# Performance work log

Hardware: AMD Instinct MI355X
Metric: run time of the kernel (lower is better)

Reference implementation:

```python
import jax, jax.numpy as jnp
import numpy as np

N_EMBD = 1024
N_HEAD = 16


def setup_inputs() -> dict:
    key = jax.random.key(0)
    k1, k2, k3 = jax.random.split(key, 3)
    x = jax.random.normal(k1, (4, 2048, N_EMBD), dtype=jnp.float32)
    w_attn = jax.random.normal(k2, (N_EMBD, 3 * N_EMBD), dtype=jnp.float32) * (N_EMBD ** -0.5)
    w_proj = jax.random.normal(k3, (N_EMBD, N_EMBD), dtype=jnp.float32) * (N_EMBD ** -0.5)
    return {"x": x, "w_attn": w_attn, "w_proj": w_proj}


def reference(x, w_attn, w_proj):
    B, T, C = x.shape
    H = N_HEAD
    D = C // H  # head dim
    qkv = x @ w_attn  # [B,T,3C]
    q, k, v = jnp.split(qkv, 3, axis=-1)
    # [B,T,C] -> [B,H,T,D]
    q = q.reshape(B, T, H, D).transpose(0, 2, 1, 3)
    k = k.reshape(B, T, H, D).transpose(0, 2, 1, 3)
    v = v.reshape(B, T, H, D).transpose(0, 2, 1, 3)
    scale = 1.0 / jnp.sqrt(jnp.asarray(D, dtype=x.dtype))
    att = jnp.einsum('bhqd,bhkd->bhqk', q, k) * scale  # [B,H,T,T]
    causal = jnp.tril(jnp.ones((T, T), dtype=bool))
    att = jnp.where(causal, att, jnp.asarray(-jnp.inf, dtype=att.dtype))
    att = jax.nn.softmax(att, axis=-1)
    y = jnp.einsum('bhqk,bhkd->bhqd', att, v)  # [B,H,T,D]
    y = y.transpose(0, 2, 1, 3).reshape(B, T, C)
    return y @ w_proj
```

## Files before the change

kernel.cpp:

```cpp
#include <hip/hip_runtime.h>
#include <math.h>


typedef unsigned short ushort_t;
typedef __attribute__((ext_vector_type(8))) short bf16x8;
typedef __attribute__((ext_vector_type(4))) float f32x4;

#define MFMA16(a, b, c) __builtin_amdgcn_mfma_f32_16x16x32_bf16((a), (b), (c), 0, 0, 0)

#define CP_ASYNC16(lds, gp)                                                        \
    __builtin_amdgcn_global_load_lds(                                              \
        (const __attribute__((address_space(1))) void*)(gp),                       \
        (__attribute__((address_space(3))) void*)(lds), 16, 0, 0)

#define SCALE2 0.1803368801111204f

__device__ __forceinline__ ushort_t bf16r(float x) {
    unsigned int u = __float_as_uint(x);
    u += 0x7FFFu + ((u >> 16) & 1u);
    return (ushort_t)(u >> 16);
}


__global__ __launch_bounds__(256) void cast_f32_bf16(const float4* __restrict__ src,
                                                     ushort4* __restrict__ dst) {
    int i = blockIdx.x * 256 + threadIdx.x;
    float4 v = src[i];
    ushort4 o;
    o.x = bf16r(v.x); o.y = bf16r(v.y); o.z = bf16r(v.z); o.w = bf16r(v.w);
    dst[i] = o;
}

__global__ __launch_bounds__(256) void transpose_cast(const float* __restrict__ src,
                                                      ushort_t* __restrict__ dst,
                                                      int R, int Cc) {
    __shared__ float tile[32][33];
    const int tx = threadIdx.x, ty = threadIdx.y;
    const int c0 = blockIdx.x * 32, r0 = blockIdx.y * 32;
#pragma unroll
    for (int i = 0; i < 4; ++i)
        tile[ty + i * 8][tx] = src[(size_t)(r0 + ty + i * 8) * Cc + c0 + tx];
    __syncthreads();
#pragma unroll
    for (int i = 0; i < 4; ++i)
        dst[(size_t)(c0 + ty + i * 8) * R + r0 + tx] = bf16r(tile[tx][ty + i * 8]);
}

__global__ __launch_bounds__(256)
void gemm_bf16(const ushort_t* __restrict__ A, const ushort_t* __restrict__ Bt,
               int K, int mode,
               ushort_t* __restrict__ Qh, ushort_t* __restrict__ Kh,
               ushort_t* __restrict__ Vt, float* __restrict__ Cout) {
    __shared__ ushort_t As[2][128 * 32];
    __shared__ ushort_t Bs[2][128 * 32];
    const int tid = threadIdx.x;
    const int l = tid & 63, w = tid >> 6;
    const int lm = l & 15, lq = l >> 4;
    const int wm = w >> 1, wn = w & 1;
    const int row0 = blockIdx.y * 128, col0 = blockIdx.x * 128;
    const f32x4 zero4 = {0.f, 0.f, 0.f, 0.f};
    const int lqs8 = (lq ^ ((lm >> 1) & 3)) * 8;

    f32x4 acc[4][4];
#pragma unroll
    for (int i = 0; i < 4; ++i)
#pragma unroll
        for (int j = 0; j < 4; ++j) acc[i][j] = zero4;

    const int srow = tid >> 2, slot = tid & 3;
    const int soff = (slot ^ ((srow >> 1) & 3)) * 8;
    const ushort_t* ga0 = A + (size_t)(row0 + srow) * K + soff;
    const ushort_t* ga1 = ga0 + (size_t)64 * K;
    const ushort_t* gb0 = Bt + (size_t)(col0 + srow) * K + soff;
    const ushort_t* gb1 = gb0 + (size_t)64 * K;

    const int aoffb = (wm * 64 + lm) * 32 + lqs8;
    const int boffb = (wn * 64 + lm) * 32 + lqs8;

    auto prefetch = [&](int k0, int dbuf) {
        CP_ASYNC16(&As[dbuf][tid * 8], ga0 + k0);
        CP_ASYNC16(&As[dbuf][(tid + 256) * 8], ga1 + k0);
        CP_ASYNC16(&Bs[dbuf][tid * 8], gb0 + k0);
        CP_ASYNC16(&Bs[dbuf][(tid + 256) * 8], gb1 + k0);
    };

    prefetch(0, 0);
    const int niter = K >> 5;
    for (int it = 0; it < niter; ++it) {
        const int buf = it & 1;
        __syncthreads();
        if (it + 1 < niter) prefetch((it + 1) << 5, buf ^ 1);

        bf16x8 af[4], bfr[4];
#pragma unroll
        for (int i = 0; i < 4; ++i)
            af[i] = *(const bf16x8*)(As[buf] + aoffb + i * (16 * 32));
#pragma unroll
        for (int j = 0; j < 4; ++j)
            bfr[j] = *(const bf16x8*)(Bs[buf] + boffb + j * (16 * 32));
#pragma unroll
        for (int i = 0; i < 4; ++i)
#pragma unroll
            for (int j = 0; j < 4; ++j)
                acc[i][j] = MFMA16(af[i], bfr[j], acc[i][j]);
    }

#pragma unroll
    for (int i = 0; i < 4; ++i) {
#pragma unroll
        for (int j = 0; j < 4; ++j) {
#pragma unroll
            for (int reg = 0; reg < 4; ++reg) {
                const int rr = row0 + wm * 64 + i * 16 + lq * 4 + reg;
                const int cc = col0 + wn * 64 + j * 16 + lm;
                const float v = acc[i][j][reg];
                if (mode == 1) {
                    Cout[(size_t)rr * 1024 + cc] = v;
                } else {
                    const int b = rr >> 11, t = rr & 2047;
                    if (cc < 1024) {
                        const int h = cc >> 6, d = cc & 63;
                        Qh[((size_t)(b * 16 + h) * 2048 + t) * 64 + d] =
                            bf16r(v * SCALE2);
                    } else if (cc < 2048) {
                        const int c2 = cc - 1024, h = c2 >> 6, d = c2 & 63;
                        Kh[((size_t)(b * 16 + h) * 2048 + t) * 64 + d] = bf16r(v);
                    } else {
                        const int c2 = cc - 2048, h = c2 >> 6, d = c2 & 63;
                        Vt[((size_t)(b * 16 + h) * 64 + d) * 2048 + t] = bf16r(v);
                    }
                }
            }
        }
    }
}

__global__ __launch_bounds__(256, 4)
void attn_mfma(const ushort_t* __restrict__ Qh, const ushort_t* __restrict__ Kh,
               const ushort_t* __restrict__ Vt, ushort_t* __restrict__ Y) {
    __shared__ ushort_t Ks[2][4096];
    __shared__ ushort_t Vs[2][4096];
    __shared__ ushort_t Ps[4][1024];
    const int tid = threadIdx.x, l = tid & 63, w = tid >> 6;
    const int lm = l & 15, lq = l >> 4;
    const int bh = blockIdx.x;
    const int pr = blockIdx.y;
    const int qbA = pr, qbB = 31 - pr;
    const int b = bh >> 4, h = bh & 15;
    const f32x4 zero4 = {0.f, 0.f, 0.f, 0.f};
    const short oneb = (short)0x3F80;
    const bf16x8 onesf = {oneb, oneb, oneb, oneb, oneb, oneb, oneb, oneb};
    const int lqs8 = (lq ^ ((lm >> 1) & 3)) * 8;

    bf16x8 qf[2][2];
    {
        const ushort_t* qA = Qh + ((size_t)bh * 2048 + qbA * 64 + w * 16 + lm) * 64 + lq * 8;
        const ushort_t* qB = Qh + ((size_t)bh * 2048 + qbB * 64 + w * 16 + lm) * 64 + lq * 8;
        qf[0][0] = *(const bf16x8*)(qA);
        qf[0][1] = *(const bf16x8*)(qA + 32);
        qf[1][0] = *(const bf16x8*)(qB);
        qf[1][1] = *(const bf16x8*)(qB + 32);
    }

    f32x4 O[2][4], Ol[2];
#pragma unroll
    for (int q = 0; q < 2; ++q) {
        Ol[q] = zero4;
#pragma unroll
        for (int i = 0; i < 4; ++i) O[q][i] = zero4;
    }

    const int srow = tid >> 2, slot = tid & 3;
    const int srcoff = ((slot ^ ((srow >> 1) & 3)) * 8);
    const ushort_t* gKr = Kh + ((size_t)bh * 2048 + srow) * 64 + srcoff;
    const ushort_t* gVr = Vt + ((size_t)bh * 64 + srow) * 2048 + srcoff;
    ushort_t* Pw = Ps[w];

    auto prefetch = [&](int jbn, int dbuf) {
        const ushort_t* gk = gKr + (size_t)jbn * 4096;
        const ushort_t* gv = gVr + jbn * 64;
        CP_ASYNC16(&Ks[dbuf][tid * 8], gk);
        CP_ASYNC16(&Ks[dbuf][2048 + tid * 8], gk + 32);
        CP_ASYNC16(&Vs[dbuf][tid * 8], gv);
        CP_ASYNC16(&Vs[dbuf][2048 + tid * 8], gv + 32);
    };

    auto process = [&](const bf16x8 (&kf)[4][2], const ushort_t* Vb,
                       const bf16x8 (&qfr)[2], f32x4 (&Or)[4], f32x4& Olr,
                       bool diag) {
        f32x4 sf[4];
#pragma unroll
        for (int n = 0; n < 4; ++n) {
            f32x4 s_acc = zero4;
            s_acc = MFMA16(qfr[0], kf[n][0], s_acc);
            s_acc = MFMA16(qfr[1], kf[n][1], s_acc);
            sf[n] = s_acc;
        }

        float p[4][4];
#pragma unroll
        for (int n = 0; n < 4; ++n)
#pragma unroll
            for (int reg = 0; reg < 4; ++reg)
                p[n][reg] = __builtin_amdgcn_exp2f(sf[n][reg]);
        if (diag) {
#pragma unroll
            for (int n = 0; n < 4; ++n) {
                const int key = n * 16 + lm;
#pragma unroll
                for (int reg = 0; reg < 4; ++reg) {
                    const int qloc = w * 16 + lq * 4 + reg;
                    if (key > qloc) p[n][reg] = 0.f;
                }
            }
        }

#pragma unroll
        for (int n = 0; n < 4; ++n) {
            const int ch = n >> 1, nn = n & 1;
#pragma unroll
            for (int reg = 0; reg < 4; ++reg) {
                const int r = lq * 4 + reg;
                const int ss = (nn * 2 + (lm >> 3)) ^ ((2 * lq + (reg >> 1)) & 3);
                const unsigned int u = __float_as_uint(p[n][reg]) + 0x8000u;
                Pw[ch * 512 + r * 32 + ss * 8 + (lm & 7)] = (ushort_t)(u >> 16);
            }
        }
        const bf16x8 pf0 = *(const bf16x8*)(Pw + lm * 32 + lqs8);
        const bf16x8 pf1 = *(const bf16x8*)(Pw + 512 + lm * 32 + lqs8);

#pragma unroll
        for (int dn = 0; dn < 4; ++dn) {
            const bf16x8 vf0 = *(const bf16x8*)(Vb + (dn * 16 + lm) * 32 + lqs8);
            const bf16x8 vf1 = *(const bf16x8*)(Vb + 2048 + (dn * 16 + lm) * 32 + lqs8);
            Or[dn] = MFMA16(pf0, vf0, Or[dn]);
            Or[dn] = MFMA16(pf1, vf1, Or[dn]);
        }
        Olr = MFMA16(pf0, onesf, Olr);
        Olr = MFMA16(pf1, onesf, Olr);
    };

    prefetch(0, 0);
    for (int jb = 0; jb <= qbB; ++jb) {
        const int buf = jb & 1;
        __syncthreads();
        if (jb < qbB) prefetch(jb + 1, buf ^ 1);

        const ushort_t* Kb = Ks[buf];
        const ushort_t* Vb = Vs[buf];
        bf16x8 kf[4][2];
#pragma unroll
        for (int n = 0; n < 4; ++n) {
            kf[n][0] = *(const bf16x8*)(Kb + (n * 16 + lm) * 32 + lqs8);
            kf[n][1] = *(const bf16x8*)(Kb + 2048 + (n * 16 + lm) * 32 + lqs8);
        }

        process(kf, Vb, qf[1], O[1], Ol[1], jb == qbB);
        if (jb <= qbA)
            process(kf, Vb, qf[0], O[0], Ol[0], jb == qbA);
    }

#pragma unroll
    for (int qs = 0; qs < 2; ++qs) {
        const int tq = (qs ? qbB : qbA) * 64;
#pragma unroll
        for (int reg = 0; reg < 4; ++reg) {
            const float inv = 1.f / Ol[qs][reg];
            const size_t row = (size_t)b * 2048 + tq + w * 16 + lq * 4 + reg;
#pragma unroll
            for (int dn = 0; dn < 4; ++dn)
                Y[row * 1024 + h * 64 + dn * 16 + lm] = bf16r(O[qs][dn][reg] * inv);
        }
    }
}


extern "C" void kernel_launch(void* const* d_in, const int* in_sizes, int n_in,
                              void* d_out, int out_size, void* d_ws, size_t ws_size,
                              hipStream_t stream) {
    const float* x      = (const float*)d_in[0];
    const float* w_attn = (const float*)d_in[1];
    const float* w_proj = (const float*)d_in[2];
    float* out = (float*)d_out;

    char* ws = (char*)d_ws;
    ushort_t* xb   = (ushort_t*)(ws);
    ushort_t* watT = (ushort_t*)(ws + 16777216);
    ushort_t* wpjT = (ushort_t*)(ws + 23068672);
    ushort_t* Qh   = (ushort_t*)(ws + 25165824);
    ushort_t* Kh   = (ushort_t*)(ws + 41943040);
    ushort_t* Vt   = (ushort_t*)(ws + 58720256);
    ushort_t* Y    = (ushort_t*)(ws + 75497472);

    hipLaunchKernelGGL(cast_f32_bf16, dim3(8192), dim3(256), 0, stream,
                       (const float4*)x, (ushort4*)xb);
    hipLaunchKernelGGL(transpose_cast, dim3(96, 32), dim3(32, 8), 0, stream,
                       w_attn, watT, 1024, 3072);
    hipLaunchKernelGGL(transpose_cast, dim3(32, 32), dim3(32, 8), 0, stream,
                       w_proj, wpjT, 1024, 1024);

    hipLaunchKernelGGL(gemm_bf16, dim3(24, 64), dim3(256), 0, stream,
                       xb, watT, 1024, 0, Qh, Kh, Vt, (float*)nullptr);

    hipLaunchKernelGGL(attn_mfma, dim3(64, 16), dim3(256), 0, stream,
                       Qh, Kh, Vt, Y);

    hipLaunchKernelGGL(gemm_bf16, dim3(8, 64), dim3(256), 0, stream,
                       Y, wpjT, 1024, 1, (ushort_t*)nullptr, (ushort_t*)nullptr,
                       (ushort_t*)nullptr, out);
}
```

Before: 295.2 us.

## Keep attention probabilities in registers via transposed QK^T and permlane swaps

Computes S transposed by swapping the MFMA operand order, so each lane holds the scores for its own query row. The probabilities are packed to bf16 with v_cvt_pk_bf16_f32 and rearranged into the PV A-operand layout with permlane32/16 swaps, which removes the per-warp LDS scratch buffer and its write/read round trip. It also raises wave priority around the MFMA blocks with s_setprio. Packed conversion uses the hardware rounding mode instead of the old add-0x8000 truncation, and correctness depends on the permlane fragment mapping being exact.

Measured after the change: 261.7 us. -11.3%, faster.

```diff
diff --git a/kernel.cpp b/kernel.cpp
--- a/kernel.cpp
+++ b/kernel.cpp
@@ -19,6 +19,18 @@
     unsigned int u = __float_as_uint(x);
     u += 0x7FFFu + ((u >> 16) & 1u);
     return (ushort_t)(u >> 16);
+}
+
+__device__ __forceinline__ unsigned cvt_pk_bf16(float lo, float hi) {
+    unsigned r;
+    asm("v_cvt_pk_bf16_f32 %0, %1, %2" : "=v"(r) : "v"(lo), "v"(hi));
+    return r;
+}
+__device__ __forceinline__ void pl32_swap(unsigned& a, unsigned& c) {
+    asm("v_permlane32_swap_b32 %0, %1" : "+v"(a), "+v"(c));
+}
+__device__ __forceinline__ void pl16_swap(unsigned& a, unsigned& c) {
+    asm("v_permlane16_swap_b32 %0, %1" : "+v"(a), "+v"(c));
 }
 
 
@@ -140,7 +152,6 @@
                const ushort_t* __restrict__ Vt, ushort_t* __restrict__ Y) {
     __shared__ ushort_t Ks[2][4096];
     __shared__ ushort_t Vs[2][4096];
-    __shared__ ushort_t Ps[4][1024];
     const int tid = threadIdx.x, l = tid & 63, w = tid >> 6;
     const int lm = l & 15, lq = l >> 4;
     const int bh = blockIdx.x;
@@ -174,7 +185,6 @@
     const int srcoff = ((slot ^ ((srow >> 1) & 3)) * 8);
     const ushort_t* gKr = Kh + ((size_t)bh * 2048 + srow) * 64 + srcoff;
     const ushort_t* gVr = Vt + ((size_t)bh * 64 + srow) * 2048 + srcoff;
-    ushort_t* Pw = Ps[w];
 
     auto prefetch = [&](int jbn, int dbuf) {
         const ushort_t* gk = gKr + (size_t)jbn * 4096;
@@ -188,47 +198,57 @@
     auto process = [&](const bf16x8 (&kf)[4][2], const ushort_t* Vb,
                        const bf16x8 (&qfr)[2], f32x4 (&Or)[4], f32x4& Olr,
                        bool diag) {
-        f32x4 sf[4];
+        f32x4 st[4];
+        __builtin_amdgcn_s_setprio(1);
 #pragma unroll
         for (int n = 0; n < 4; ++n) {
             f32x4 s_acc = zero4;
-            s_acc = MFMA16(qfr[0], kf[n][0], s_acc);
-            s_acc = MFMA16(qfr[1], kf[n][1], s_acc);
-            sf[n] = s_acc;
-        }
+            s_acc = MFMA16(kf[n][0], qfr[0], s_acc);
+            s_acc = MFMA16(kf[n][1], qfr[1], s_acc);
+            st[n] = s_acc;
+        }
+        __builtin_amdgcn_s_setprio(0);
 
         float p[4][4];
 #pragma unroll
         for (int n = 0; n < 4; ++n)
 #pragma unroll
             for (int reg = 0; reg < 4; ++reg)
-                p[n][reg] = __builtin_amdgcn_exp2f(sf[n][reg]);
+                p[n][reg] = __builtin_amdgcn_exp2f(st[n][reg]);
         if (diag) {
-#pragma unroll
-            for (int n = 0; n < 4; ++n) {
-                const int key = n * 16 + lm;
-#pragma unroll
-                for (int reg = 0; reg < 4; ++reg) {
-                    const int qloc = w * 16 + lq * 4 + reg;
-                    if (key > qloc) p[n][reg] = 0.f;
-                }
-            }
-        }
-
+            const int qloc = w * 16 + lm;
+#pragma unroll
+            for (int n = 0; n < 4; ++n)
+#pragma unroll
+                for (int reg = 0; reg < 4; ++reg)
+                    if (n * 16 + lq * 4 + reg > qloc) p[n][reg] = 0.f;
+        }
+
+        unsigned cpk[4][2];
 #pragma unroll
         for (int n = 0; n < 4; ++n) {
-            const int ch = n >> 1, nn = n & 1;
-#pragma unroll
-            for (int reg = 0; reg < 4; ++reg) {
-                const int r = lq * 4 + reg;
-                const int ss = (nn * 2 + (lm >> 3)) ^ ((2 * lq + (reg >> 1)) & 3);
-                const unsigned int u = __float_as_uint(p[n][reg]) + 0x8000u;
-                Pw[ch * 512 + r * 32 + ss * 8 + (lm & 7)] = (ushort_t)(u >> 16);
-            }
-        }
-        const bf16x8 pf0 = *(const bf16x8*)(Pw + lm * 32 + lqs8);
-        const bf16x8 pf1 = *(const bf16x8*)(Pw + 512 + lm * 32 + lqs8);
-
+            cpk[n][0] = cvt_pk_bf16(p[n][0], p[n][1]);
+            cpk[n][1] = cvt_pk_bf16(p[n][2], p[n][3]);
+        }
+
+        union U8 { unsigned u[4]; bf16x8 v; };
+        bf16x8 pf0, pf1;
+        {
+            unsigned z00 = cpk[0][0], z10 = cpk[1][0];
+            unsigned z01 = cpk[0][1], z11 = cpk[1][1];
+            pl32_swap(z00, z10); pl16_swap(z00, z10);
+            pl32_swap(z01, z11); pl16_swap(z01, z11);
+            U8 t0; t0.u[0] = z00; t0.u[1] = z01; t0.u[2] = z10; t0.u[3] = z11;
+            pf0 = t0.v;
+            unsigned y00 = cpk[2][0], y10 = cpk[3][0];
+            unsigned y01 = cpk[2][1], y11 = cpk[3][1];
+            pl32_swap(y00, y10); pl16_swap(y00, y10);
+            pl32_swap(y01, y11); pl16_swap(y01, y11);
+            U8 t1; t1.u[0] = y00; t1.u[1] = y01; t1.u[2] = y10; t1.u[3] = y11;
+            pf1 = t1.v;
+        }
+
+        __builtin_amdgcn_s_setprio(1);
 #pragma unroll
         for (int dn = 0; dn < 4; ++dn) {
             const bf16x8 vf0 = *(const bf16x8*)(Vb + (dn * 16 + lm) * 32 + lqs8);
@@ -238,6 +258,7 @@
         }
         Olr = MFMA16(pf0, onesf, Olr);
         Olr = MFMA16(pf1, onesf, Olr);
+        __builtin_amdgcn_s_setprio(0);
     };
 
     prefetch(0, 0);
```
